# Performance work log

Hardware: AMD Instinct MI355X
Metric: run time of the kernel (lower is better)

## Reference

```python
import jax, jax.numpy as jnp
from jax import lax
import numpy as np

PATCH = 8
THRESHOLD = 0.2  # learned per-layer threshold, at init value


def conv2d(x, w, b, pad):
    # x: (N,C,H,W), w: (O,I,kh,kw)
    y = lax.conv_general_dilated(x, w, (1, 1), [(pad, pad), (pad, pad)],
                                 dimension_numbers=('NCHW', 'OIHW', 'NCHW'))
    return y + b[None, :, None, None]


def extract_patches(X, p):
    # Appends 4 positional channels, then splits into non-overlapping p x p patches.
    B, C, H, W = X.shape
    gy, gx = jnp.meshgrid(jnp.linspace(0.0, 1.0, H), jnp.linspace(0.0, 1.0, W), indexing='ij')
    pos = jnp.stack([gx, gy, jnp.sin(jnp.pi * gx), jnp.sin(jnp.pi * gy)]).astype(X.dtype)  # (4,H,W)
    Xc = jnp.concatenate([X, jnp.broadcast_to(pos[None], (B, 4, H, W))], axis=1)  # (B,C+4,H,W)
    h, w = H // p, W // p
    Xp = Xc.reshape(B, C + 4, h, p, w, p).transpose(0, 2, 4, 1, 3, 5).reshape(B, h * w, C + 4, p, p)
    return Xp, h, w


def _forward(X,
             proj_w0, proj_b0, exp_w0, exp_b0, fin_w0, fin_b0,
             proj_w1, proj_b1, exp_w1, exp_b1, fin_w1, fin_b1,
             proj_w2, proj_b2, exp_w2, exp_b2, fin_w2, fin_b2,
             proj_w3, proj_b3, exp_w3, exp_b3, fin_w3, fin_b3,
             router_w, router_b, lin_w, lin_b):
    layers = [
        (proj_w0, proj_b0, exp_w0, exp_b0, fin_w0, fin_b0),
        (proj_w1, proj_b1, exp_w1, exp_b1, fin_w1, fin_b1),
        (proj_w2, proj_b2, exp_w2, exp_b2, fin_w2, fin_b2),
        (proj_w3, proj_b3, exp_w3, exp_b3, fin_w3, fin_b3),
    ]
    for (pw, pb, ew, eb, fw, fb) in layers:
        Xp, h, w = extract_patches(X, PATCH)        # (B,P,C,p,p)
        B, P, C, pH, pW = Xp.shape
        flat = Xp.reshape(B * P, C, pH, pW)
        # router: conv-proj -> global avg pool -> linear -> softmax
        pooled = conv2d(flat, pw, pb, 1).mean(axis=(2, 3))                 # (BP, 8)
        scores = jax.nn.softmax(pooled @ router_w.T + router_b, axis=-1)  # (BP, E)
        scores = scores.reshape(B, P, -1)                                  # (B,P,E)
        # all experts as one grouped conv: (E,Co,C,3,3) -> (E*Co,C,3,3)
        E, Co = ew.shape[0], ew.shape[1]
        eo = conv2d(flat, ew.reshape(E * Co, C, 3, 3), eb.reshape(E * Co), 1)
        eo = jax.nn.relu(eo).reshape(B, P, E, Co, pH, pW)
        # expert is skipped unless some patch score exceeds the layer threshold
        gate = (scores.max(axis=(0, 1)) > THRESHOLD).astype(X.dtype)        # (E,)
        comb = jnp.einsum('bpechw,bpe->bpchw', eo, scores * gate[None, None, :])
        img = comb.reshape(B, h, w, Co, pH, pW).transpose(0, 3, 1, 4, 2, 5)
        img = img.reshape(B, Co, h * pH, w * pW)
        X = conv2d(img, fw, fb, 4)  # 1x1 conv, padding=4 -> H,W grow by 8
    return X.reshape(X.shape[0], -1) @ lin_w.T + lin_b


def setup_inputs() -> dict:
    key = jax.random.key(0)
    ks = iter(jax.random.split(key, 64))

    def nrm(shape, fan_in):
        return jax.random.normal(next(ks), shape, jnp.float32) / np.sqrt(fan_in)

    d = {"X": jax.random.normal(next(ks), (16, 3, 64, 64), jnp.float32)}
    cin = [7, 68, 68, 132]   # expert/key input channels per layer (prev out + 4 pos)
    cout = [64, 64, 128, 128]
    E = 4
    for l in range(4):
        d[f"proj_w{l}"] = nrm((8, cin[l], 3, 3), cin[l] * 9)
        d[f"proj_b{l}"] = jnp.zeros((8,), jnp.float32)
        d[f"exp_w{l}"] = nrm((E, cout[l], cin[l], 3, 3), cin[l] * 9)
        d[f"exp_b{l}"] = jnp.zeros((E, cout[l]), jnp.float32)
        d[f"fin_w{l}"] = nrm((cout[l], cout[l], 1, 1), cout[l])
        d[f"fin_b{l}"] = jnp.zeros((cout[l],), jnp.float32)
    d["router_w"] = nrm((E, 8), 8)
    d["router_b"] = jnp.zeros((E,), jnp.float32)
    feat = 128 * 96 * 96  # final (B,128,96,96) flattened
    d["lin_w"] = nrm((10, feat), feat)
    d["lin_b"] = jnp.zeros((10,), jnp.float32)
    return d


def reference(X,
              proj_w0, proj_b0, exp_w0, exp_b0, fin_w0, fin_b0,
              proj_w1, proj_b1, exp_w1, exp_b1, fin_w1, fin_b1,
              proj_w2, proj_b2, exp_w2, exp_b2, fin_w2, fin_b2,
              proj_w3, proj_b3, exp_w3, exp_b3, fin_w3, fin_b3,
              router_w, router_b, lin_w, lin_b):
    return _forward(X,
                    proj_w0, proj_b0, exp_w0, exp_b0, fin_w0, fin_b0,
                    proj_w1, proj_b1, exp_w1, exp_b1, fin_w1, fin_b1,
                    proj_w2, proj_b2, exp_w2, exp_b2, fin_w2, fin_b2,
                    proj_w3, proj_b3, exp_w3, exp_b3, fin_w3, fin_b3,
                    router_w, router_b, lin_w, lin_b)
```

## Files before the change

kernel.cpp:

```cpp
#include <hip/hip_runtime.h>
#include <math.h>

#define NB 16
#define NE 4
#define THRESH 0.2f
#define LIN_NS 64

typedef __attribute__((ext_vector_type(8))) _Float16 f16x8;
typedef __attribute__((ext_vector_type(4))) float f32x4;
typedef unsigned short u16;
typedef unsigned int u32;

__device__ inline u16 f16bits(float v) { _Float16 h = (_Float16)v; return __builtin_bit_cast(u16, h); }
__device__ inline u32 pack2(float a, float b) { return (u32)f16bits(a) | ((u32)f16bits(b) << 16); }
__device__ inline float unpk(u32 x, int hi) {
    return (float)__builtin_bit_cast(_Float16, (u16)(hi ? (x >> 16) : (x & 0xffff)));
}

__global__ void repack_all_kernel(const float* __restrict__ ew, const float* __restrict__ fw,
    u16* __restrict__ Wm, u16* __restrict__ Wp, u16* __restrict__ fW,
    int CO, int CIN, int CINp, int C) {
    const int M = NE * CO;
    const int n1 = 9 * M * CINp, n2 = M * 64, n3 = CO * CO;
    const int n = n1 + n2 + n3;
    for (int i = blockIdx.x * blockDim.x + threadIdx.x; i < n; i += gridDim.x * blockDim.x) {
        if (i < n1) {
            int k = i % CINp; int t = i / CINp; int m = t % M; int ij = t / M;
            float v = (k < CIN) ? ew[(m * C + k) * 9 + ij] : 0.f;
            Wm[i] = f16bits(v);
        } else if (i < n1 + n2) {
            int j = i - n1; int kp = j & 63; int m = j >> 6;
            float v = 0.f;
            if (kp < 36) { int pc = kp / 9, ij = kp % 9; v = ew[(m * C + CIN + pc) * 9 + ij]; }
            Wp[j] = f16bits(v);
        } else {
            int j = i - n1 - n2;
            fW[j] = f16bits(fw[j]);
        }
    }
}

template<int CIN, int C>
__global__ __launch_bounds__(256) void router_kernel(
    const float* __restrict__ X, const float* __restrict__ pw, const float* __restrict__ pb,
    const float* __restrict__ rw, const float* __restrict__ rb,
    float* __restrict__ scores, int H, int W, int nP)
{
    __shared__ float S[4][C * 9 + 8];
    const int wv = threadIdx.x >> 6;
    const int lane = threadIdx.x & 63;
    const int bp = blockIdx.x * 4 + wv;
    const int P = nP * nP;
    const int b = bp / P, pi = bp % P;
    const int py = pi / nP, px = pi % nP;
    const int h = lane >> 3, w = lane & 7;
    const int gy = py * 8 + h, gx = px * 8 + w;
    float* Sw = S[wv];
    for (int c = 0; c < C; ++c) {
        float v;
        if (c < CIN) {
            v = X[(((size_t)b * CIN + c) * H + gy) * W + gx];
        } else {
            float t = (c == CIN || c == CIN + 2) ? gx * (1.f / (W - 1)) : gy * (1.f / (H - 1));
            v = (c >= CIN + 2) ? sinf(3.14159265358979323846f * t) : t;
        }
        float r = v;
        r += __shfl_xor(r, 1); r += __shfl_xor(r, 2); r += __shfl_xor(r, 4);
        float cc = v;
        cc += __shfl_xor(cc, 8); cc += __shfl_xor(cc, 16); cc += __shfl_xor(cc, 32);
        float T = r;
        T += __shfl_xor(T, 8); T += __shfl_xor(T, 16); T += __shfl_xor(T, 32);
        float R0 = __shfl(r, 0), R7 = __shfl(r, 56);
        float C0 = __shfl(cc, 0), C7 = __shfl(cc, 7);
        float x00 = __shfl(v, 0), x07 = __shfl(v, 7);
        float x70 = __shfl(v, 56), x77 = __shfl(v, 63);
        if (lane < 9) {
            int i = lane / 3, j = lane % 3;
            float s = T;
            if (i == 0) s -= R7; else if (i == 2) s -= R0;
            if (j == 0) s -= C7; else if (j == 2) s -= C0;
            if (i == 0 && j == 0) s += x77;
            else if (i == 0 && j == 2) s += x70;
            else if (i == 2 && j == 0) s += x07;
            else if (i == 2 && j == 2) s += x00;
            Sw[c * 9 + lane] = s;
        }
    }
    __syncthreads();
    if (lane < 8) {
        const int o = lane;
        float acc = 0.f;
        for (int c = 0; c < C; ++c) {
            #pragma unroll
            for (int ij = 0; ij < 9; ++ij)
                acc += pw[(o * C + c) * 9 + ij] * Sw[c * 9 + ij];
        }
        Sw[C * 9 + o] = acc * (1.f / 64.f) + pb[o];
    }
    __syncthreads();
    if (lane == 0) {
        float lg[NE];
        float m = -1e30f;
        #pragma unroll
        for (int e = 0; e < NE; ++e) {
            float a = rb[e];
            #pragma unroll
            for (int o = 0; o < 8; ++o) a += Sw[C * 9 + o] * rw[e * 8 + o];
            lg[e] = a;
            m = fmaxf(m, a);
        }
        float ssum = 0.f;
        #pragma unroll
        for (int e = 0; e < NE; ++e) { lg[e] = __expf(lg[e] - m); ssum += lg[e]; }
        float inv = 1.f / ssum;
        #pragma unroll
        for (int e = 0; e < NE; ++e) scores[bp * NE + e] = lg[e] * inv;
    }
}

__global__ __launch_bounds__(256) void gate_kernel(const float* __restrict__ scores, int BP,
                                                   float* __restrict__ gate)
{
    __shared__ float sm[4][NE];
    float m[NE] = {-1e30f, -1e30f, -1e30f, -1e30f};
    for (int i = threadIdx.x; i < BP; i += 256) {
        #pragma unroll
        for (int e = 0; e < NE; ++e) m[e] = fmaxf(m[e], scores[i * NE + e]);
    }
    #pragma unroll
    for (int e = 0; e < NE; ++e) {
        float v = m[e];
        for (int o = 32; o; o >>= 1) v = fmaxf(v, __shfl_xor(v, o));
        m[e] = v;
    }
    int wv = threadIdx.x >> 6, lane = threadIdx.x & 63;
    if (lane == 0) {
        #pragma unroll
        for (int e = 0; e < NE; ++e) sm[wv][e] = m[e];
    }
    __syncthreads();
    if (threadIdx.x == 0) {
        #pragma unroll
        for (int e = 0; e < NE; ++e) {
            float mx = fmaxf(fmaxf(sm[0][e], sm[1][e]), fmaxf(sm[2][e], sm[3][e]));
            gate[e] = (mx > THRESH) ? 1.f : 0.f;
        }
    }
}

__global__ __launch_bounds__(256) void border_kernel(float* __restrict__ Xn,
                                                     const float* __restrict__ fb,
                                                     int CO, int H, int W)
{
    const int Hout = H + 8, Wout = W + 8;
    const int nb = 16 * H + 64;
    const long total = (long)NB * CO * nb;
    for (long i = (long)blockIdx.x * blockDim.x + threadIdx.x; i < total;
         i += (long)gridDim.x * blockDim.x) {
        int j = (int)(i % nb); long t = i / nb; int o = (int)(t % CO); int b = (int)(t / CO);
        int y, x;
        if (j < 4 * Wout)       { y = j / Wout;             x = j % Wout; }
        else if (j < 8 * Wout)  { int j2 = j - 4 * Wout; y = H + 4 + j2 / Wout; x = j2 % Wout; }
        else                    { int j3 = j - 8 * Wout; y = 4 + j3 / 8;
                                  int c8 = j3 % 8; x = (c8 < 4) ? c8 : W + 4 + (c8 - 4); }
        Xn[(((size_t)b * CO + o) * Hout + y) * Wout + x] = fb[o];
    }
}

template<int CIN, int CINp, int CO>
__global__ __launch_bounds__(512, 4) void expert_fused_kernel(
    const float* __restrict__ X,
    const u16* __restrict__ Wm, const u16* __restrict__ Wp, const u16* __restrict__ fW,
    const float* __restrict__ eb, const float* __restrict__ fb,
    const float* __restrict__ scores, const float* __restrict__ gate,
    float* __restrict__ Xn, int H, int W, int nP)
{
    constexpr int M = NE * CO;
    constexpr int KSM = CINp / 32;
    constexpr int SP = CINp + 8;
    constexpr int PIP = 72;
    constexpr int CP = CO + 8;
    constexpr bool FAT = (CO == 128);
    constexpr int NT = FAT ? 8 : 4;
    constexpr int EPP = FAT ? 2 : 4;
    constexpr int NPASS = NE / EPP;
    constexpr int PATW = 2 * 100 * SP;
    constexpr int POSW = 2 * 64 * PIP;
    constexpr int COMBW = 2 * 64 * CP;
    constexpr int SMW = (PATW + POSW > COMBW) ? (PATW + POSW) : COMBW;

    __shared__ __align__(16) u16 smem[SMW];
    __shared__ float pospix[2][4][64];
    u16* pat = smem;
    u16* posim = smem + PATW;
    u16* comb = smem;

    const int P = nP * nP;
    const int bp0 = blockIdx.x * 2, bp1 = bp0 + 1;
    const int b0 = bp0 / P, pi0 = bp0 % P, py0 = pi0 / nP, px0 = pi0 % nP;
    const int b1 = bp1 / P, pi1 = bp1 % P, py1 = pi1 / nP, px1 = pi1 % nP;
    const int tid = threadIdx.x;
    const int Hout = H + 8, Wout = W + 8;

    for (int i = tid; i < 100 * SP; i += 512) ((u32*)pat)[i] = 0;
    {
        int g = tid >> 8, r = tid & 255, pc = r >> 6, p = r & 63;
        int gy = (g ? py1 : py0) * 8 + (p >> 3), gx = (g ? px1 : px0) * 8 + (p & 7);
        float t = (pc == 0 || pc == 2) ? gx * (1.f / (W - 1)) : gy * (1.f / (H - 1));
        pospix[g][pc][p] = (pc >= 2) ? sinf(3.14159265358979323846f * t) : t;
    }
    __syncthreads();
    for (int i = tid; i < 2 * CIN * 16; i += 512) {
        int g = i / (CIN * 16), j = i % (CIN * 16);
        int c = j >> 4, q = j & 15, h = q >> 1, w4 = (q & 1) * 4;
        int bb = g ? b1 : b0, py = g ? py1 : py0, px = g ? px1 : px0;
        const float4 v = *(const float4*)&X[(((size_t)bb * CIN + c) * H + py * 8 + h) * W + px * 8 + w4];
        int base = g * 100 * SP + c;
        pat[base + ((h + 1) * 10 + (w4 + 1)) * SP] = f16bits(v.x);
        pat[base + ((h + 1) * 10 + (w4 + 2)) * SP] = f16bits(v.y);
        pat[base + ((h + 1) * 10 + (w4 + 3)) * SP] = f16bits(v.z);
        pat[base + ((h + 1) * 10 + (w4 + 4)) * SP] = f16bits(v.w);
    }
    for (int i = tid; i < 2 * 64 * 64; i += 512) {
        int g = i >> 12, r = i & 4095, pix = r >> 6, kp = r & 63;
        float v = 0.f;
        if (kp < 36) {
            int pc = kp / 9, ij = kp % 9;
            int hh = (pix >> 3) + ij / 3 - 1, ww = (pix & 7) + ij % 3 - 1;
            if (hh >= 0 && hh < 8 && ww >= 0 && ww < 8) v = pospix[g][pc][hh * 8 + ww];
        }
        posim[g * 64 * PIP + pix * PIP + kp] = f16bits(v);
    }
    __syncthreads();

    const int lane = tid & 63, wv = tid >> 6;
    const int colp = lane & 15, kg = lane >> 4;
    const int cot = FAT ? wv : (wv & 3);
    const int gO = FAT ? 0 : (wv >> 2);
    const int co0 = cot * 16;

    int prow[NT];
    #pragma unroll
    for (int nt = 0; nt < NT; ++nt) {
        int g = FAT ? (nt >> 2) : gO;
        int pix = (nt & 3) * 16 + colp;
        prow[nt] = g * 100 * SP + ((pix >> 3) * 10 + (pix & 7)) * SP;
    }

    u32 pk[NT][2];

    #pragma unroll
    for (int pass = 0; pass < NPASS; ++pass) {
        f32x4 acc[EPP][NT];
        #pragma unroll
        for (int ee = 0; ee < EPP; ++ee)
            #pragma unroll
            for (int nt = 0; nt < NT; ++nt) acc[ee][nt] = (f32x4){0.f, 0.f, 0.f, 0.f};

        int aoff[EPP];
        #pragma unroll
        for (int ee = 0; ee < EPP; ++ee)
            aoff[ee] = ((pass * EPP + ee) * CO + co0 + colp) * CINp + kg * 8;

        for (int ij = 0; ij < 9; ++ij) {
            const int tap = (ij / 3) * 10 + (ij % 3);
            const int wb = ij * M * CINp;
            #pragma unroll
            for (int ks = 0; ks < KSM; ++ks) {
                f16x8 Ah[EPP];
                #pragma unroll
                for (int ee = 0; ee < EPP; ++ee)
                    Ah[ee] = *(const f16x8*)(Wm + wb + aoff[ee] + ks * 32);
                __builtin_amdgcn_s_setprio(1);
                #pragma unroll
                for (int nt = 0; nt < NT; ++nt) {
                    f16x8 Bv = *(const f16x8*)&pat[prow[nt] + tap * SP + ks * 32 + kg * 8];
                    #pragma unroll
                    for (int ee = 0; ee < EPP; ++ee)
                        acc[ee][nt] = __builtin_amdgcn_mfma_f32_16x16x32_f16(Ah[ee], Bv, acc[ee][nt], 0, 0, 0);
                }
                __builtin_amdgcn_s_setprio(0);
            }
        }
        #pragma unroll
        for (int ks = 0; ks < 2; ++ks) {
            f16x8 Ah[EPP];
            #pragma unroll
            for (int ee = 0; ee < EPP; ++ee)
                Ah[ee] = *(const f16x8*)(Wp + ((pass * EPP + ee) * CO + co0 + colp) * 64 + ks * 32 + kg * 8);
            __builtin_amdgcn_s_setprio(1);
            #pragma unroll
            for (int nt = 0; nt < NT; ++nt) {
                int g = FAT ? (nt >> 2) : gO;
                int pix = (nt & 3) * 16 + colp;
                f16x8 Bv = *(const f16x8*)&posim[g * 64 * PIP + pix * PIP + ks * 32 + kg * 8];
                #pragma unroll
                for (int ee = 0; ee < EPP; ++ee)
                    acc[ee][nt] = __builtin_amdgcn_mfma_f32_16x16x32_f16(Ah[ee], Bv, acc[ee][nt], 0, 0, 0);
            }
            __builtin_amdgcn_s_setprio(0);
        }

        float sgA[2][EPP], ebvP[EPP][4];
        #pragma unroll
        for (int ee = 0; ee < EPP; ++ee) {
            int e = pass * EPP + ee;
            float gv = gate[e];
            sgA[0][ee] = scores[bp0 * NE + e] * gv;
            sgA[1][ee] = scores[bp1 * NE + e] * gv;
            #pragma unroll
            for (int r = 0; r < 4; ++r) ebvP[ee][r] = eb[e * CO + co0 + kg * 4 + r];
        }
        #pragma unroll
        for (int nt = 0; nt < NT; ++nt) {
            const int g = FAT ? (nt >> 2) : gO;
            #pragma unroll
            for (int rr = 0; rr < 2; ++rr) {
                float cv0 = 0.f, cv1 = 0.f;
                #pragma unroll
                for (int ee = 0; ee < EPP; ++ee) {
                    float s = sgA[g][ee];
                    cv0 += s * fmaxf(acc[ee][nt][2 * rr]     + ebvP[ee][2 * rr],     0.f);
                    cv1 += s * fmaxf(acc[ee][nt][2 * rr + 1] + ebvP[ee][2 * rr + 1], 0.f);
                }
                if (NPASS == 2 && pass == 1) {
                    cv0 += unpk(pk[nt][rr], 0);
                    cv1 += unpk(pk[nt][rr], 1);
                }
                pk[nt][rr] = pack2(cv0, cv1);
            }
        }
    }

    __syncthreads();

    #pragma unroll
    for (int nt = 0; nt < NT; ++nt) {
        const int g = FAT ? (nt >> 2) : gO;
        int pix = (nt & 3) * 16 + colp;
        uint2 q;
        q.x = pk[nt][0];
        q.y = pk[nt][1];
        *(uint2*)&comb[g * 64 * CP + pix * CP + co0 + kg * 4] = q;
    }
    __syncthreads();

    const int o0 = co0;
    f32x4 accF[NT];
    #pragma unroll
    for (int nt = 0; nt < NT; ++nt) accF[nt] = (f32x4){0.f, 0.f, 0.f, 0.f};
    #pragma unroll
    for (int ks = 0; ks < CO / 32; ++ks) {
        int ao = (o0 + colp) * CO + ks * 32 + kg * 8;
        f16x8 ah = *(const f16x8*)(fW + ao);
        __builtin_amdgcn_s_setprio(1);
        #pragma unroll
        for (int nt = 0; nt < NT; ++nt) {
            int g = FAT ? (nt >> 2) : gO;
            int pix = (nt & 3) * 16 + colp;
            f16x8 bv = *(const f16x8*)&comb[g * 64 * CP + pix * CP + ks * 32 + kg * 8];
            accF[nt] = __builtin_amdgcn_mfma_f32_16x16x32_f16(ah, bv, accF[nt], 0, 0, 0);
        }
        __builtin_amdgcn_s_setprio(0);
    }
    float fbv[4];
    #pragma unroll
    for (int r = 0; r < 4; ++r) fbv[r] = fb[o0 + kg * 4 + r];
    #pragma unroll
    for (int nt = 0; nt < NT; ++nt) {
        const int g = FAT ? (nt >> 2) : gO;
        int pix = (nt & 3) * 16 + colp;
        int bb = g ? b1 : b0, py = g ? py1 : py0, px = g ? px1 : px0;
        int gy = py * 8 + (pix >> 3) + 4, gx = px * 8 + (pix & 7) + 4;
        #pragma unroll
        for (int r = 0; r < 4; ++r) {
            int o = o0 + kg * 4 + r;
            Xn[(((size_t)bb * CO + o) * Hout + gy) * Wout + gx] = accF[nt][r] + fbv[r];
        }
    }
}

__global__ __launch_bounds__(256) void linear_part_kernel(
    const float* __restrict__ Xf, const float* __restrict__ lw, float* __restrict__ part)
{
    const int feat = 128 * 96 * 96;
    const int CH = feat / LIN_NS;
    const int b = blockIdx.x / LIN_NS, s = blockIdx.x % LIN_NS;
    const float4* xa = (const float4*)(Xf + (size_t)b * feat + (size_t)s * CH);
    const float* wbase = lw + (size_t)s * CH;
    float acc[10];
    #pragma unroll
    for (int o = 0; o < 10; ++o) acc[o] = 0.f;
    const int n4 = CH / 4;
    for (int i = threadIdx.x; i < n4; i += 256) {
        float4 xv = xa[i];
        #pragma unroll
        for (int o = 0; o < 10; ++o) {
            float4 wv = *(const float4*)(wbase + (size_t)o * feat + i * 4);
            acc[o] += xv.x * wv.x + xv.y * wv.y + xv.z * wv.z + xv.w * wv.w;
        }
    }
    #pragma unroll
    for (int o = 0; o < 10; ++o)
        for (int m = 32; m; m >>= 1) acc[o] += __shfl_xor(acc[o], m);
    __shared__ float sm[4][10];
    int wv = threadIdx.x >> 6, lane = threadIdx.x & 63;
    if (lane == 0) {
        #pragma unroll
        for (int o = 0; o < 10; ++o) sm[wv][o] = acc[o];
    }
    __syncthreads();
    if (threadIdx.x < 10)
        part[(b * LIN_NS + s) * 10 + threadIdx.x] =
            sm[0][threadIdx.x] + sm[1][threadIdx.x] + sm[2][threadIdx.x] + sm[3][threadIdx.x];
}

__global__ __launch_bounds__(256) void linear_reduce_kernel(
    const float* __restrict__ part, const float* __restrict__ lb, float* __restrict__ out)
{
    int i = threadIdx.x;
    if (i < 160) {
        int b = i / 10, o = i % 10;
        float a = lb[o];
        for (int s = 0; s < LIN_NS; ++s) a += part[(b * LIN_NS + s) * 10 + o];
        out[i] = a;
    }
}

template<int CIN, int CINp, int CO>
static void run_layer(const float* Xin, int H, int nP, const float* const* Lw,
                      const float* rw, const float* rb,
                      const u16* Wm, const u16* Wp, const u16* fW,
                      float* scores, float* gate, float* Xn, hipStream_t stream)
{
    const int W = H;
    const int BP = NB * nP * nP;
    const float* pw = Lw[0]; const float* pb = Lw[1];
    const float* ebias = Lw[3];
    const float* fb = Lw[5];

    router_kernel<CIN, CIN + 4><<<BP / 4, 256, 0, stream>>>(Xin, pw, pb, rw, rb, scores, H, W, nP);
    gate_kernel<<<1, 256, 0, stream>>>(scores, BP, gate);
    border_kernel<<<2048, 256, 0, stream>>>(Xn, fb, CO, H, W);
    expert_fused_kernel<CIN, CINp, CO><<<BP / 2, 512, 0, stream>>>(
        Xin, Wm, Wp, fW, ebias, fb, scores, gate, Xn, H, W, nP);
}

extern "C" void kernel_launch(void* const* d_in, const int* in_sizes, int n_in,
                              void* d_out, int out_size, void* d_ws, size_t ws_size,
                              hipStream_t stream)
{
    const float* X0 = (const float*)d_in[0];
    const float* L[4][6];
    for (int l = 0; l < 4; ++l)
        for (int k = 0; k < 6; ++k) L[l][k] = (const float*)d_in[1 + l * 6 + k];
    const float* rw = (const float*)d_in[25];
    const float* rb = (const float*)d_in[26];
    const float* lw = (const float*)d_in[27];
    const float* lb = (const float*)d_in[28];

    char* ws = (char*)d_ws;
    const size_t XA_B = 63438848;
    const size_t XB_B = 75497472;
    float* XA = (float*)(ws);
    float* XB = (float*)(ws + XA_B);
    char* wp = ws + XA_B + XB_B;
    const int cfg_CO[4]   = {64, 64, 128, 128};
    const int cfg_CINp[4] = {32, 64, 64, 128};
    u16 *Wm[4], *Wp[4], *fW[4];
    for (int l = 0; l < 4; ++l) {
        int M = NE * cfg_CO[l];
        Wm[l] = (u16*)wp;            wp += (size_t)9 * M * cfg_CINp[l] * 2;
        Wp[l] = (u16*)wp;            wp += (size_t)M * 64 * 2;
        fW[l] = (u16*)wp;            wp += (size_t)cfg_CO[l] * cfg_CO[l] * 2;
    }
    float* scores = (float*)wp;
    float* gate = scores + 1936 * 4;
    float* lpart = gate + 64;

    const int cfg_CIN[4] = {3, 64, 64, 128};
    for (int l = 0; l < 4; ++l)
        repack_all_kernel<<<512, 256, 0, stream>>>(L[l][2], L[l][4], Wm[l], Wp[l], fW[l],
                                                   cfg_CO[l], cfg_CIN[l], cfg_CINp[l], cfg_CIN[l] + 4);

    run_layer<3,   32,  64>(X0, 64,  8, L[0], rw, rb, Wm[0], Wp[0], fW[0], scores, gate, XA, stream);
    run_layer<64,  64,  64>(XA, 72,  9, L[1], rw, rb, Wm[1], Wp[1], fW[1], scores, gate, XB, stream);
    run_layer<64,  64, 128>(XB, 80, 10, L[2], rw, rb, Wm[2], Wp[2], fW[2], scores, gate, XA, stream);
    run_layer<128, 128, 128>(XA, 88, 11, L[3], rw, rb, Wm[3], Wp[3], fW[3], scores, gate, XB, stream);

    linear_part_kernel<<<16 * LIN_NS, 256, 0, stream>>>(XB, lw, lpart);
    linear_reduce_kernel<<<1, 256, 0, stream>>>(lpart, lb, (float*)d_out);
}
```

Before: 841.7 us.

## Restructure expert conv loop to iterate patches per pass with all experts

The wide (CO=128) expert kernel used to split its four experts across two passes, holding the combined result between passes as packed fp16 and re-adding it. It now runs one pass per patch, covering all four experts at once, with B-fragments loaded once per k-step and reused across experts. Each patch's combined output goes straight to shared memory. This drops the fp16 partial-sum round trip and reuses activation loads more. In exchange it adds a barrier per pass, can grow shared memory when the combine buffer does not fit in the dead patch area, and changes the register pressure profile.

```diff
diff --git a/kernel.cpp b/kernel.cpp
--- a/kernel.cpp
+++ b/kernel.cpp
@@ -13,9 +13,6 @@
 
 __device__ inline u16 f16bits(float v) { _Float16 h = (_Float16)v; return __builtin_bit_cast(u16, h); }
 __device__ inline u32 pack2(float a, float b) { return (u32)f16bits(a) | ((u32)f16bits(b) << 16); }
-__device__ inline float unpk(u32 x, int hi) {
-    return (float)__builtin_bit_cast(_Float16, (u16)(hi ? (x >> 16) : (x & 0xffff)));
-}
 
 __global__ void repack_all_kernel(const float* __restrict__ ew, const float* __restrict__ fw,
     u16* __restrict__ Wm, u16* __restrict__ Wp, u16* __restrict__ fW,
@@ -182,18 +179,17 @@
     constexpr int CP = CO + 8;
     constexpr bool FAT = (CO == 128);
     constexpr int NT = FAT ? 8 : 4;
-    constexpr int EPP = FAT ? 2 : 4;
-    constexpr int NPASS = NE / EPP;
+    constexpr int NPASS = FAT ? 2 : 1;
     constexpr int PATW = 2 * 100 * SP;
     constexpr int POSW = 2 * 64 * PIP;
-    constexpr int COMBW = 2 * 64 * CP;
-    constexpr int SMW = (PATW + POSW > COMBW) ? (PATW + POSW) : COMBW;
+    constexpr bool EXTRA = FAT && (64 * CP > 100 * SP);
+    constexpr int C1OFF = FAT ? (EXTRA ? (PATW + POSW) : 100 * SP) : 64 * CP;
+    constexpr int SMW = PATW + POSW + (EXTRA ? 64 * CP : 0);
 
     __shared__ __align__(16) u16 smem[SMW];
     __shared__ float pospix[2][4][64];
     u16* pat = smem;
     u16* posim = smem + PATW;
-    u16* comb = smem;
 
     const int P = nP * nP;
     const int bp0 = blockIdx.x * 2, bp1 = bp0 + 1;
@@ -239,109 +235,93 @@
     const int gO = FAT ? 0 : (wv >> 2);
     const int co0 = cot * 16;
 
-    int prow[NT];
-    #pragma unroll
-    for (int nt = 0; nt < NT; ++nt) {
-        int g = FAT ? (nt >> 2) : gO;
-        int pix = (nt & 3) * 16 + colp;
-        prow[nt] = g * 100 * SP + ((pix >> 3) * 10 + (pix & 7)) * SP;
-    }
-
-    u32 pk[NT][2];
-
     #pragma unroll
     for (int pass = 0; pass < NPASS; ++pass) {
-        f32x4 acc[EPP][NT];
-        #pragma unroll
-        for (int ee = 0; ee < EPP; ++ee)
-            #pragma unroll
-            for (int nt = 0; nt < NT; ++nt) acc[ee][nt] = (f32x4){0.f, 0.f, 0.f, 0.f};
-
-        int aoff[EPP];
-        #pragma unroll
-        for (int ee = 0; ee < EPP; ++ee)
-            aoff[ee] = ((pass * EPP + ee) * CO + co0 + colp) * CINp + kg * 8;
+        const int g = FAT ? (1 - pass) : gO;
+        const int bpg = g ? bp1 : bp0;
+
+        f32x4 acc[NE][4];
+        #pragma unroll
+        for (int e = 0; e < NE; ++e)
+            #pragma unroll
+            for (int nt = 0; nt < 4; ++nt) acc[e][nt] = (f32x4){0.f, 0.f, 0.f, 0.f};
+
+        int prow[4];
+        #pragma unroll
+        for (int nt = 0; nt < 4; ++nt) {
+            int pix = nt * 16 + colp;
+            prow[nt] = g * 100 * SP + ((pix >> 3) * 10 + (pix & 7)) * SP;
+        }
 
         for (int ij = 0; ij < 9; ++ij) {
             const int tap = (ij / 3) * 10 + (ij % 3);
             const int wb = ij * M * CINp;
             #pragma unroll
             for (int ks = 0; ks < KSM; ++ks) {
-                f16x8 Ah[EPP];
+                f16x8 Bv[4];
                 #pragma unroll
-                for (int ee = 0; ee < EPP; ++ee)
-                    Ah[ee] = *(const f16x8*)(Wm + wb + aoff[ee] + ks * 32);
+                for (int nt = 0; nt < 4; ++nt)
+                    Bv[nt] = *(const f16x8*)&pat[prow[nt] + tap * SP + ks * 32 + kg * 8];
+                #pragma unroll
+                for (int e = 0; e < NE; ++e) {
+                    f16x8 Ah = *(const f16x8*)(Wm + wb + (e * CO + co0 + colp) * CINp + ks * 32 + kg * 8);
+                    __builtin_amdgcn_s_setprio(1);
+                    #pragma unroll
+                    for (int nt = 0; nt < 4; ++nt)
+                        acc[e][nt] = __builtin_amdgcn_mfma_f32_16x16x32_f16(Ah, Bv[nt], acc[e][nt], 0, 0, 0);
+                    __builtin_amdgcn_s_setprio(0);
+                }
+            }
+        }
+        #pragma unroll
+        for (int ks = 0; ks < 2; ++ks) {
+            f16x8 Bv[4];
+            #pragma unroll
+            for (int nt = 0; nt < 4; ++nt) {
+                int pix = nt * 16 + colp;
+                Bv[nt] = *(const f16x8*)&posim[g * 64 * PIP + pix * PIP + ks * 32 + kg * 8];
+            }
+            #pragma unroll
+            for (int e = 0; e < NE; ++e) {
+                f16x8 Ah = *(const f16x8*)(Wp + (e * CO + co0 + colp) * 64 + ks * 32 + kg * 8);
                 __builtin_amdgcn_s_setprio(1);
                 #pragma unroll
-                for (int nt = 0; nt < NT; ++nt) {
-                    f16x8 Bv = *(const f16x8*)&pat[prow[nt] + tap * SP + ks * 32 + kg * 8];
-                    #pragma unroll
-                    for (int ee = 0; ee < EPP; ++ee)
-                        acc[ee][nt] = __builtin_amdgcn_mfma_f32_16x16x32_f16(Ah[ee], Bv, acc[ee][nt], 0, 0, 0);
-                }
+                for (int nt = 0; nt < 4; ++nt)
+                    acc[e][nt] = __builtin_amdgcn_mfma_f32_16x16x32_f16(Ah, Bv[nt], acc[e][nt], 0, 0, 0);
                 __builtin_amdgcn_s_setprio(0);
             }
         }
-        #pragma unroll
-        for (int ks = 0; ks < 2; ++ks) {
-            f16x8 Ah[EPP];
-            #pragma unroll
-            for (int ee = 0; ee < EPP; ++ee)
-                Ah[ee] = *(const f16x8*)(Wp + ((pass * EPP + ee) * CO + co0 + colp) * 64 + ks * 32 + kg * 8);
-            __builtin_amdgcn_s_setprio(1);
-            #pragma unroll
-            for (int nt = 0; nt < NT; ++nt) {
-                int g = FAT ? (nt >> 2) : gO;
-                int pix = (nt & 3) * 16 + colp;
-                f16x8 Bv = *(const f16x8*)&posim[g * 64 * PIP + pix * PIP + ks * 32 + kg * 8];
-                #pragma unroll
-                for (int ee = 0; ee < EPP; ++ee)
-                    acc[ee][nt] = __builtin_amdgcn_mfma_f32_16x16x32_f16(Ah[ee], Bv, acc[ee][nt], 0, 0, 0);
-            }
-            __builtin_amdgcn_s_setprio(0);
-        }
-
-        float sgA[2][EPP], ebvP[EPP][4];
-        #pragma unroll
-        for (int ee = 0; ee < EPP; ++ee) {
-            int e = pass * EPP + ee;
-            float gv = gate[e];
-            sgA[0][ee] = scores[bp0 * NE + e] * gv;
-            sgA[1][ee] = scores[bp1 * NE + e] * gv;
-            #pragma unroll
-            for (int r = 0; r < 4; ++r) ebvP[ee][r] = eb[e * CO + co0 + kg * 4 + r];
-        }
-        #pragma unroll
-        for (int nt = 0; nt < NT; ++nt) {
-            const int g = FAT ? (nt >> 2) : gO;
+
+        float sg[NE], ebv[NE][4];
+        #pragma unroll
+        for (int e = 0; e < NE; ++e) {
+            sg[e] = scores[bpg * NE + e] * gate[e];
+            #pragma unroll
+            for (int r = 0; r < 4; ++r) ebv[e][r] = eb[e * CO + co0 + kg * 4 + r];
+        }
+        u32 pk[4][2];
+        #pragma unroll
+        for (int nt = 0; nt < 4; ++nt) {
             #pragma unroll
             for (int rr = 0; rr < 2; ++rr) {
                 float cv0 = 0.f, cv1 = 0.f;
                 #pragma unroll
-                for (int ee = 0; ee < EPP; ++ee) {
-                    float s = sgA[g][ee];
-                    cv0 += s * fmaxf(acc[ee][nt][2 * rr]     + ebvP[ee][2 * rr],     0.f);
-                    cv1 += s * fmaxf(acc[ee][nt][2 * rr + 1] + ebvP[ee][2 * rr + 1], 0.f);
-                }
-                if (NPASS == 2 && pass == 1) {
-                    cv0 += unpk(pk[nt][rr], 0);
-                    cv1 += unpk(pk[nt][rr], 1);
+                for (int e = 0; e < NE; ++e) {
+                    cv0 += sg[e] * fmaxf(acc[e][nt][2 * rr]     + ebv[e][2 * rr],     0.f);
+                    cv1 += sg[e] * fmaxf(acc[e][nt][2 * rr + 1] + ebv[e][2 * rr + 1], 0.f);
                 }
                 pk[nt][rr] = pack2(cv0, cv1);
             }
         }
-    }
-
-    __syncthreads();
-
-    #pragma unroll
-    for (int nt = 0; nt < NT; ++nt) {
-        const int g = FAT ? (nt >> 2) : gO;
-        int pix = (nt & 3) * 16 + colp;
-        uint2 q;
-        q.x = pk[nt][0];
-        q.y = pk[nt][1];
-        *(uint2*)&comb[g * 64 * CP + pix * CP + co0 + kg * 4] = q;
+
+        __syncthreads();
+        u16* cg = smem + (g ? C1OFF : 0);
+        #pragma unroll
+        for (int nt = 0; nt < 4; ++nt) {
+            int pix = nt * 16 + colp;
+            uint2 q; q.x = pk[nt][0]; q.y = pk[nt][1];
+            *(uint2*)&cg[pix * CP + co0 + kg * 4] = q;
+        }
     }
     __syncthreads();
 
@@ -351,14 +331,14 @@
     for (int nt = 0; nt < NT; ++nt) accF[nt] = (f32x4){0.f, 0.f, 0.f, 0.f};
     #pragma unroll
     for (int ks = 0; ks < CO / 32; ++ks) {
-        int ao = (o0 + colp) * CO + ks * 32 + kg * 8;
-        f16x8 ah = *(const f16x8*)(fW + ao);
+        f16x8 ah = *(const f16x8*)(fW + (o0 + colp) * CO + ks * 32 + kg * 8);
         __builtin_amdgcn_s_setprio(1);
         #pragma unroll
         for (int nt = 0; nt < NT; ++nt) {
             int g = FAT ? (nt >> 2) : gO;
             int pix = (nt & 3) * 16 + colp;
-            f16x8 bv = *(const f16x8*)&comb[g * 64 * CP + pix * CP + ks * 32 + kg * 8];
+            const u16* cg = smem + (g ? C1OFF : 0);
+            f16x8 bv = *(const f16x8*)&cg[pix * CP + ks * 32 + kg * 8];
             accF[nt] = __builtin_amdgcn_mfma_f32_16x16x32_f16(ah, bv, accF[nt], 0, 0, 0);
         }
         __builtin_amdgcn_s_setprio(0);
```

After: 1.108 ms. 1.32x slower.
